# Kernel optimization log

Measured on AMD Instinct MI355X. Metric: run time of the kernel, lower is better.

## Reference

```python
import jax, jax.numpy as jnp
import numpy as np

DIM = 4096
N_EXPERTS = 64
TOP_K = 2
TOKENS = 16384


def setup_inputs() -> dict:
    key = jax.random.key(0)
    k1, k2 = jax.random.split(key)
    x = jax.random.normal(k1, (TOKENS, DIM), dtype=jnp.float32)
    # nn.Linear weight is [out_features, in_features] = [n_experts, dim]
    w_gate = jax.random.normal(k2, (N_EXPERTS, DIM), dtype=jnp.float32) * (1.0 / np.sqrt(DIM))
    return {"x": x, "w_gate": w_gate}


def reference(x, w_gate):
    # logits: [tokens, n_experts]
    logits = jnp.einsum("td,ed->te", x, w_gate)
    gates = jax.nn.softmax(logits, axis=-1)
    topk_vals, topk_idx = jax.lax.top_k(gates, TOP_K)
    return (gates, topk_vals, topk_idx)
```

## Files before the change

### kernel.cpp

```cpp
#include <hip/hip_runtime.h>
#include <hip/hip_bf16.h>
#include <stdint.h>

typedef float f32x4 __attribute__((ext_vector_type(4)));
typedef __attribute__((address_space(3))) uint32_t lds_u32_t;
typedef __attribute__((address_space(1))) const uint32_t glb_u32_t;

#define TOKENS 16384
#define DIM    4096
#define NEXP   64
#define TPB    32
#define KC     64
#define GSZ    (TOKENS*NEXP)
#define VSZ    (TOKENS*2)

__global__ __launch_bounds__(256, 2)
void router_kernel(const float* __restrict__ x,
                   const float* __restrict__ w,
                   float* __restrict__ out)
{
    __shared__ f32x4 xs4[TPB*KC/4];
    __shared__ f32x4 ws4[NEXP*KC/4];

    const int tid  = threadIdx.x;
    const int tr   = tid >> 4;
    const int ec   = tid & 15;
    const int tok0 = blockIdx.x * TPB;

    const f32x4 vzero = {0.f, 0.f, 0.f, 0.f};
    f32x4 acc[2][4];
#pragma unroll
    for (int i = 0; i < 2; ++i)
#pragma unroll
        for (int j = 0; j < 4; ++j) acc[i][j] = vzero;

    float* xsf = (float*)xs4;
    float* wsf = (float*)ws4;

    for (int k0 = 0; k0 < DIM; k0 += KC) {
        __syncthreads();
#pragma unroll
        for (int n = 0; n < 2; ++n) {
            int idx   = tid + n*256;
            int row   = idx >> 4;
            int slot  = idx & 15;
            int kslot = slot ^ ((row >> 1) & 15);
            const float* gp = x + (size_t)(tok0 + row)*DIM + k0 + kslot*4;
            float* lp = xsf + idx*4;
            __builtin_amdgcn_global_load_lds((glb_u32_t*)gp, (lds_u32_t*)lp, 16, 0, 0);
        }
#pragma unroll
        for (int n = 0; n < 4; ++n) {
            int idx   = tid + n*256;
            int e     = idx >> 4;
            int slot  = idx & 15;
            int kslot = slot ^ ((e >> 2) & 15);
            const float* gp = w + (size_t)e*DIM + k0 + kslot*4;
            float* lp = wsf + idx*4;
            __builtin_amdgcn_global_load_lds((glb_u32_t*)gp, (lds_u32_t*)lp, 16, 0, 0);
        }
        __syncthreads();

#pragma unroll
        for (int s = 0; s < 16; ++s) {
            const int sx = s ^ tr;
            const int sw = s ^ ec;
            f32x4 xv0 = xs4[(2*tr + 0)*16 + sx];
            f32x4 xv1 = xs4[(2*tr + 1)*16 + sx];
            f32x4 wv0 = ws4[(4*ec + 0)*16 + sw];
            f32x4 wv1 = ws4[(4*ec + 1)*16 + sw];
            f32x4 wv2 = ws4[(4*ec + 2)*16 + sw];
            f32x4 wv3 = ws4[(4*ec + 3)*16 + sw];
            acc[0][0] += xv0*wv0;  acc[0][1] += xv0*wv1;
            acc[0][2] += xv0*wv2;  acc[0][3] += xv0*wv3;
            acc[1][0] += xv1*wv0;  acc[1][1] += xv1*wv1;
            acc[1][2] += xv1*wv2;  acc[1][3] += xv1*wv3;
        }
    }

#pragma unroll
    for (int i = 0; i < 2; ++i) {
        const int t = tok0 + 2*tr + i;
        float l[4];
#pragma unroll
        for (int j = 0; j < 4; ++j) {
            f32x4 a = acc[i][j];
            l[j] = (a[0] + a[1]) + (a[2] + a[3]);
        }
        float m = fmaxf(fmaxf(l[0], l[1]), fmaxf(l[2], l[3]));
#pragma unroll
        for (int off = 1; off < 16; off <<= 1)
            m = fmaxf(m, __shfl_xor(m, off));
        float e0 = expf(l[0]-m), e1 = expf(l[1]-m), e2 = expf(l[2]-m), e3 = expf(l[3]-m);
        float ssum = (e0+e1) + (e2+e3);
#pragma unroll
        for (int off = 1; off < 16; off <<= 1)
            ssum += __shfl_xor(ssum, off);
        float inv = 1.0f / ssum;
        f32x4 g = {e0*inv, e1*inv, e2*inv, e3*inv};
        *(f32x4*)(out + (size_t)t*NEXP + 4*ec) = g;

        float v1 = l[0]; int i1 = 4*ec;
        float v2 = -__builtin_inff(); int i2 = 1 << 30;
#pragma unroll
        for (int j = 1; j < 4; ++j) {
            float lv = l[j]; int li = 4*ec + j;
            bool b1 = (lv > v1) || (lv == v1 && li < i1);
            bool b2 = (lv > v2) || (lv == v2 && li < i2);
            float pv1 = v1; int pi1 = i1;
            v1 = b1 ? lv : v1;   i1 = b1 ? li : i1;
            v2 = b1 ? pv1 : (b2 ? lv : v2);
            i2 = b1 ? pi1 : (b2 ? li : i2);
        }
#pragma unroll
        for (int off = 1; off < 16; off <<= 1) {
            float ov1 = __shfl_xor(v1, off); int oi1 = __shfl_xor(i1, off);
            float ov2 = __shfl_xor(v2, off); int oi2 = __shfl_xor(i2, off);
            bool afirst = (v1 > ov1) || (v1 == ov1 && i1 < oi1);
            float nv1, nv2; int ni1, ni2;
            if (afirst) {
                nv1 = v1; ni1 = i1;
                bool b = (v2 > ov1) || (v2 == ov1 && i2 < oi1);
                nv2 = b ? v2 : ov1;  ni2 = b ? i2 : oi1;
            } else {
                nv1 = ov1; ni1 = oi1;
                bool b = (ov2 > v1) || (ov2 == v1 && oi2 < i1);
                nv2 = b ? ov2 : v1;  ni2 = b ? oi2 : i1;
            }
            v1 = nv1; i1 = ni1; v2 = nv2; i2 = ni2;
        }
        if (ec == 0) {
            out[GSZ + 2*(size_t)t + 0] = expf(v1 - m) * inv;
            out[GSZ + 2*(size_t)t + 1] = expf(v2 - m) * inv;
            out[GSZ + VSZ + 2*(size_t)t + 0] = (float)i1;
            out[GSZ + VSZ + 2*(size_t)t + 1] = (float)i2;
        }
    }
}

extern "C" void kernel_launch(void* const* d_in, const int* in_sizes, int n_in,
                              void* d_out, int out_size, void* d_ws, size_t ws_size,
                              hipStream_t stream) {
    (void)in_sizes; (void)n_in; (void)d_ws; (void)ws_size; (void)out_size;
    const float* x = (const float*)d_in[0];
    const float* w = (const float*)d_in[1];
    float* out     = (float*)d_out;
    dim3 grid(TOKENS / TPB);
    dim3 block(256);
    router_kernel<<<grid, block, 0, stream>>>(x, w, out);
}
```

Before: 424.6 us.

## Compute router logits with split-fp16 MFMA and double-buffered LDS

```diff
diff --git a/kernel.cpp b/kernel.cpp
--- a/kernel.cpp
+++ b/kernel.cpp
@@ -1,140 +1,192 @@
 #include <hip/hip_runtime.h>
-#include <hip/hip_bf16.h>
 #include <stdint.h>
 
 typedef float f32x4 __attribute__((ext_vector_type(4)));
-typedef __attribute__((address_space(3))) uint32_t lds_u32_t;
-typedef __attribute__((address_space(1))) const uint32_t glb_u32_t;
+typedef _Float16 f16;
+typedef _Float16 f16x8 __attribute__((ext_vector_type(8)));
 
 #define TOKENS 16384
 #define DIM    4096
 #define NEXP   64
-#define TPB    32
+#define BM     32
 #define KC     64
+#define NCHUNK (DIM/KC)
 #define GSZ    (TOKENS*NEXP)
 #define VSZ    (TOKENS*2)
+#define BUFSZ  24576
+#define LSTR   68
+
+__device__ __forceinline__ void split8(f32x4 a, f32x4 b, f16x8& h, f16x8& l) {
+#pragma unroll
+    for (int i = 0; i < 4; ++i) {
+        float v = a[i]; f16 hi = (f16)v;
+        h[i] = hi; l[i] = (f16)(v - (float)hi);
+    }
+#pragma unroll
+    for (int i = 0; i < 4; ++i) {
+        float v = b[i]; f16 hi = (f16)v;
+        h[4+i] = hi; l[4+i] = (f16)(v - (float)hi);
+    }
+}
 
 __global__ __launch_bounds__(256, 2)
 void router_kernel(const float* __restrict__ x,
                    const float* __restrict__ w,
                    float* __restrict__ out)
 {
-    __shared__ f32x4 xs4[TPB*KC/4];
-    __shared__ f32x4 ws4[NEXP*KC/4];
+    __shared__ unsigned char smem[2*BUFSZ];
 
     const int tid  = threadIdx.x;
-    const int tr   = tid >> 4;
-    const int ec   = tid & 15;
-    const int tok0 = blockIdx.x * TPB;
-
-    const f32x4 vzero = {0.f, 0.f, 0.f, 0.f};
-    f32x4 acc[2][4];
-#pragma unroll
-    for (int i = 0; i < 2; ++i)
-#pragma unroll
-        for (int j = 0; j < 4; ++j) acc[i][j] = vzero;
-
-    float* xsf = (float*)xs4;
-    float* wsf = (float*)ws4;
-
-    for (int k0 = 0; k0 < DIM; k0 += KC) {
-        __syncthreads();
-#pragma unroll
-        for (int n = 0; n < 2; ++n) {
-            int idx   = tid + n*256;
-            int row   = idx >> 4;
-            int slot  = idx & 15;
-            int kslot = slot ^ ((row >> 1) & 15);
-            const float* gp = x + (size_t)(tok0 + row)*DIM + k0 + kslot*4;
-            float* lp = xsf + idx*4;
-            __builtin_amdgcn_global_load_lds((glb_u32_t*)gp, (lds_u32_t*)lp, 16, 0, 0);
-        }
-#pragma unroll
-        for (int n = 0; n < 4; ++n) {
-            int idx   = tid + n*256;
-            int e     = idx >> 4;
-            int slot  = idx & 15;
-            int kslot = slot ^ ((e >> 2) & 15);
-            const float* gp = w + (size_t)e*DIM + k0 + kslot*4;
-            float* lp = wsf + idx*4;
-            __builtin_amdgcn_global_load_lds((glb_u32_t*)gp, (lds_u32_t*)lp, 16, 0, 0);
-        }
-        __syncthreads();
-
-#pragma unroll
-        for (int s = 0; s < 16; ++s) {
-            const int sx = s ^ tr;
-            const int sw = s ^ ec;
-            f32x4 xv0 = xs4[(2*tr + 0)*16 + sx];
-            f32x4 xv1 = xs4[(2*tr + 1)*16 + sx];
-            f32x4 wv0 = ws4[(4*ec + 0)*16 + sw];
-            f32x4 wv1 = ws4[(4*ec + 1)*16 + sw];
-            f32x4 wv2 = ws4[(4*ec + 2)*16 + sw];
-            f32x4 wv3 = ws4[(4*ec + 3)*16 + sw];
-            acc[0][0] += xv0*wv0;  acc[0][1] += xv0*wv1;
-            acc[0][2] += xv0*wv2;  acc[0][3] += xv0*wv3;
-            acc[1][0] += xv1*wv0;  acc[1][1] += xv1*wv1;
-            acc[1][2] += xv1*wv2;  acc[1][3] += xv1*wv3;
-        }
-    }
-
-#pragma unroll
-    for (int i = 0; i < 2; ++i) {
-        const int t = tok0 + 2*tr + i;
-        float l[4];
-#pragma unroll
-        for (int j = 0; j < 4; ++j) {
-            f32x4 a = acc[i][j];
-            l[j] = (a[0] + a[1]) + (a[2] + a[3]);
-        }
-        float m = fmaxf(fmaxf(l[0], l[1]), fmaxf(l[2], l[3]));
-#pragma unroll
-        for (int off = 1; off < 16; off <<= 1)
-            m = fmaxf(m, __shfl_xor(m, off));
-        float e0 = expf(l[0]-m), e1 = expf(l[1]-m), e2 = expf(l[2]-m), e3 = expf(l[3]-m);
-        float ssum = (e0+e1) + (e2+e3);
-#pragma unroll
-        for (int off = 1; off < 16; off <<= 1)
-            ssum += __shfl_xor(ssum, off);
-        float inv = 1.0f / ssum;
-        f32x4 g = {e0*inv, e1*inv, e2*inv, e3*inv};
-        *(f32x4*)(out + (size_t)t*NEXP + 4*ec) = g;
-
-        float v1 = l[0]; int i1 = 4*ec;
-        float v2 = -__builtin_inff(); int i2 = 1 << 30;
-#pragma unroll
-        for (int j = 1; j < 4; ++j) {
-            float lv = l[j]; int li = 4*ec + j;
-            bool b1 = (lv > v1) || (lv == v1 && li < i1);
-            bool b2 = (lv > v2) || (lv == v2 && li < i2);
-            float pv1 = v1; int pi1 = i1;
-            v1 = b1 ? lv : v1;   i1 = b1 ? li : i1;
-            v2 = b1 ? pv1 : (b2 ? lv : v2);
-            i2 = b1 ? pi1 : (b2 ? li : i2);
-        }
-#pragma unroll
-        for (int off = 1; off < 16; off <<= 1) {
-            float ov1 = __shfl_xor(v1, off); int oi1 = __shfl_xor(i1, off);
-            float ov2 = __shfl_xor(v2, off); int oi2 = __shfl_xor(i2, off);
-            bool afirst = (v1 > ov1) || (v1 == ov1 && i1 < oi1);
-            float nv1, nv2; int ni1, ni2;
-            if (afirst) {
-                nv1 = v1; ni1 = i1;
-                bool b = (v2 > ov1) || (v2 == ov1 && i2 < oi1);
-                nv2 = b ? v2 : ov1;  ni2 = b ? i2 : oi1;
-            } else {
-                nv1 = ov1; ni1 = oi1;
-                bool b = (ov2 > v1) || (ov2 == v1 && oi2 < i1);
-                nv2 = b ? ov2 : v1;  ni2 = b ? oi2 : i1;
+    const int tok0 = blockIdx.x * BM;
+
+    const int xrow = tid >> 3, xks = tid & 7;
+    const int we   = tid >> 2, wq  = tid & 3;
+
+    const float* xg = x + (size_t)(tok0 + xrow)*DIM + xks*8;
+    const float* wg = w + (size_t)we*DIM + wq*16;
+
+    const int lane = tid & 63;
+    const int wv   = tid >> 6;
+    const int mt   = wv >> 1;
+    const int ntb  = (wv & 1) * 2;
+    const int frow = mt*16 + (lane & 15);
+    const int fk   = lane >> 4;
+    const int swz  = lane & 7;
+
+    f32x4 acc[2] = {{0,0,0,0},{0,0,0,0}};
+
+    f32x4 xr0, xr1, wr0, wr1, wr2, wr3;
+    xr0 = ((const f32x4*)xg)[0];  xr1 = ((const f32x4*)xg)[1];
+    wr0 = ((const f32x4*)wg)[0];  wr1 = ((const f32x4*)wg)[1];
+    wr2 = ((const f32x4*)wg)[2];  wr3 = ((const f32x4*)wg)[3];
+
+    auto cw = [&](unsigned char* base) {
+        f16* XH = (f16*)base;
+        f16* XL = XH + BM*KC;
+        f16* WH = XL + BM*KC;
+        f16* WL = WH + NEXP*KC;
+        f16x8 h, l;
+        split8(xr0, xr1, h, l);
+        int s = xks ^ (xrow & 7);
+        *(f16x8*)(XH + xrow*KC + s*8) = h;
+        *(f16x8*)(XL + xrow*KC + s*8) = l;
+        split8(wr0, wr1, h, l);
+        s = (wq*2) ^ (we & 7);
+        *(f16x8*)(WH + we*KC + s*8) = h;
+        *(f16x8*)(WL + we*KC + s*8) = l;
+        split8(wr2, wr3, h, l);
+        s = (wq*2 + 1) ^ (we & 7);
+        *(f16x8*)(WH + we*KC + s*8) = h;
+        *(f16x8*)(WL + we*KC + s*8) = l;
+    };
+
+    cw(smem);
+
+    for (int kc = 0; kc < NCHUNK; ++kc) {
+        if (kc + 1 < NCHUNK) {
+            const float* xp = xg + (kc+1)*KC;
+            const float* wp = wg + (kc+1)*KC;
+            xr0 = ((const f32x4*)xp)[0];  xr1 = ((const f32x4*)xp)[1];
+            wr0 = ((const f32x4*)wp)[0];  wr1 = ((const f32x4*)wp)[1];
+            wr2 = ((const f32x4*)wp)[2];  wr3 = ((const f32x4*)wp)[3];
+        }
+        asm volatile("s_waitcnt lgkmcnt(0)" ::: "memory");
+        __builtin_amdgcn_s_barrier();
+
+        const unsigned char* base = smem + (size_t)(kc & 1)*BUFSZ;
+        const f16* XH = (const f16*)base;
+        const f16* XL = XH + BM*KC;
+        const f16* WH = XL + BM*KC;
+        const f16* WL = WH + NEXP*KC;
+#pragma unroll
+        for (int ks = 0; ks < 2; ++ks) {
+            const int sl = (ks*4 + fk) ^ swz;
+            f16x8 ah = *(const f16x8*)(XH + frow*KC + sl*8);
+            f16x8 al = *(const f16x8*)(XL + frow*KC + sl*8);
+#pragma unroll
+            for (int n = 0; n < 2; ++n) {
+                const int e = (ntb + n)*16 + (lane & 15);
+                f16x8 bh = *(const f16x8*)(WH + e*KC + sl*8);
+                f16x8 bl = *(const f16x8*)(WL + e*KC + sl*8);
+                acc[n] = __builtin_amdgcn_mfma_f32_16x16x32_f16(ah, bh, acc[n], 0, 0, 0);
+                acc[n] = __builtin_amdgcn_mfma_f32_16x16x32_f16(ah, bl, acc[n], 0, 0, 0);
+                acc[n] = __builtin_amdgcn_mfma_f32_16x16x32_f16(al, bh, acc[n], 0, 0, 0);
             }
-            v1 = nv1; i1 = ni1; v2 = nv2; i2 = ni2;
-        }
-        if (ec == 0) {
-            out[GSZ + 2*(size_t)t + 0] = expf(v1 - m) * inv;
-            out[GSZ + 2*(size_t)t + 1] = expf(v2 - m) * inv;
-            out[GSZ + VSZ + 2*(size_t)t + 0] = (float)i1;
-            out[GSZ + VSZ + 2*(size_t)t + 1] = (float)i2;
-        }
+        }
+        if (kc + 1 < NCHUNK) cw(smem + (size_t)((kc+1) & 1)*BUFSZ);
+    }
+
+    float* lg = (float*)smem;
+#pragma unroll
+    for (int n = 0; n < 2; ++n) {
+        const int e = (ntb + n)*16 + (lane & 15);
+#pragma unroll
+        for (int i = 0; i < 4; ++i) {
+            const int trow = mt*16 + fk*4 + i;
+            lg[trow*LSTR + e] = acc[n][i];
+        }
+    }
+    __syncthreads();
+
+    const int st = tid >> 3;
+    const int sg = tid & 7;
+    const float* rowp = lg + st*LSTR + sg*8;
+    float g[8];
+#pragma unroll
+    for (int j = 0; j < 8; ++j) g[j] = rowp[j];
+    float m = g[0];
+#pragma unroll
+    for (int j = 1; j < 8; ++j) m = fmaxf(m, g[j]);
+#pragma unroll
+    for (int off = 1; off < 8; off <<= 1) m = fmaxf(m, __shfl_xor(m, off));
+    float s = 0.f;
+#pragma unroll
+    for (int j = 0; j < 8; ++j) { g[j] = expf(g[j] - m); s += g[j]; }
+#pragma unroll
+    for (int off = 1; off < 8; off <<= 1) s += __shfl_xor(s, off);
+    const float inv = 1.0f / s;
+#pragma unroll
+    for (int j = 0; j < 8; ++j) g[j] *= inv;
+
+    const size_t t = (size_t)tok0 + st;
+    f32x4 g0 = {g[0],g[1],g[2],g[3]}, g1 = {g[4],g[5],g[6],g[7]};
+    *(f32x4*)(out + t*NEXP + sg*8)     = g0;
+    *(f32x4*)(out + t*NEXP + sg*8 + 4) = g1;
+
+    float v1 = g[0]; int i1 = sg*8;
+    float v2 = -__builtin_inff(); int i2 = 1 << 30;
+#pragma unroll
+    for (int j = 1; j < 8; ++j) {
+        float lv = g[j]; int li = sg*8 + j;
+        bool b1 = (lv > v1) || (lv == v1 && li < i1);
+        bool b2 = (lv > v2) || (lv == v2 && li < i2);
+        float pv1 = v1; int pi1 = i1;
+        v1 = b1 ? lv : v1;  i1 = b1 ? li : i1;
+        v2 = b1 ? pv1 : (b2 ? lv : v2);
+        i2 = b1 ? pi1 : (b2 ? li : i2);
+    }
+#pragma unroll
+    for (int off = 1; off < 8; off <<= 1) {
+        float ov1 = __shfl_xor(v1, off); int oi1 = __shfl_xor(i1, off);
+        float ov2 = __shfl_xor(v2, off); int oi2 = __shfl_xor(i2, off);
+        bool afirst = (v1 > ov1) || (v1 == ov1 && i1 < oi1);
+        float nv1, nv2; int ni1, ni2;
+        if (afirst) {
+            nv1 = v1; ni1 = i1;
+            bool b = (v2 > ov1) || (v2 == ov1 && i2 < oi1);
+            nv2 = b ? v2 : ov1; ni2 = b ? i2 : oi1;
+        } else {
+            nv1 = ov1; ni1 = oi1;
+            bool b = (ov2 > v1) || (ov2 == v1 && oi2 < i1);
+            nv2 = b ? ov2 : v1; ni2 = b ? oi2 : i1;
+        }
+        v1 = nv1; i1 = ni1; v2 = nv2; i2 = ni2;
+    }
+    if (sg == 0) {
+        out[GSZ + 2*t]           = v1;
+        out[GSZ + 2*t + 1]       = v2;
+        out[GSZ + VSZ + 2*t]     = (float)i1;
+        out[GSZ + VSZ + 2*t + 1] = (float)i2;
     }
 }
 
@@ -145,7 +197,7 @@
     const float* x = (const float*)d_in[0];
     const float* w = (const float*)d_in[1];
     float* out     = (float*)d_out;
-    dim3 grid(TOKENS / TPB);
+    dim3 grid(TOKENS / BM);
     dim3 block(256);
     router_kernel<<<grid, block, 0, stream>>>(x, w, out);
 }
```

Measured after the change: 380.8 us. 1.11x faster.
